# Performance work log

Measured on AMD Instinct MI355X. Metric: run time of the kernel, lower is better.

## Reference

```python
import jax, jax.numpy as jnp
import numpy as np

N_IN = 262144      # input points
N_OUT = 65536      # output voxels
NBR = 32           # neighbors per voxel (uniform ragged list here)
E = N_OUT * NBR    # total edges
CIN = 32
COUT = 32
K = 3 + 1          # kernel_size = [4,4,4]
KV = K * K * K     # 64 kernel bins
EPS = 1e-8


def window_poly6(r):
    # poly6 window on normalized distance r in [0,1]
    return jnp.clip(1.0 - r * r, 0.0, 1.0) ** 3


def ball_to_cube_radial(p):
    # radially map unit ball to unit cube [-1,1]^3 (Open3D 'ball_to_cube_radial')
    n2 = jnp.sqrt(jnp.sum(p * p, axis=-1, keepdims=True) + 1e-12)
    ninf = jnp.max(jnp.abs(p), axis=-1, keepdims=True)
    scale = jnp.where(ninf > 1e-8, n2 / jnp.maximum(ninf, 1e-8), 0.0)
    return jnp.clip(p * scale, -1.0, 1.0)


def setup_inputs() -> dict:
    key = jax.random.key(0)
    ks = jax.random.split(key, 8)
    feats = jax.random.normal(ks[0], (N_IN, CIN), jnp.float32)
    inp_points = jax.random.uniform(ks[1], (N_IN, 3), jnp.float32)
    out_points = jax.random.uniform(ks[2], (N_OUT, 3), jnp.float32)
    out_extents = jnp.array([0.2], jnp.float32)  # voxel size
    scale_compat = jax.random.uniform(ks[3], (E,), jnp.float32)
    neighbors_index = jax.random.randint(ks[4], (E,), 0, N_IN).astype(jnp.int64)
    neighbors_row_splits = (jnp.arange(N_OUT + 1) * NBR).astype(jnp.int64)
    neighbors_distance = jax.random.uniform(ks[5], (E,), jnp.float32)
    # learned params of the ContinuousConv: kernel [4,4,4,Cin,Cout] flattened, bias
    W = jax.random.normal(ks[6], (KV, CIN, COUT), jnp.float32) * 0.05
    bias = jnp.zeros((COUT,), jnp.float32)
    return dict(feats=feats, inp_points=inp_points, out_points=out_points,
                out_extents=out_extents, scale_compat=scale_compat,
                neighbors_index=neighbors_index,
                neighbors_row_splits=neighbors_row_splits,
                neighbors_distance=neighbors_distance, W=W, bias=bias)


def reference(feats, inp_points, out_points, out_extents, scale_compat,
              neighbors_index, neighbors_row_splits, neighbors_distance,
              W, bias):
    # edge -> output-voxel index from ragged row splits
    out_idx = jnp.searchsorted(neighbors_row_splits, jnp.arange(E), side='right') - 1
    # per-neighbor importance (the CConvAggregationBlock weighting)
    a = scale_compat * window_poly6(neighbors_distance)
    # relative positions normalized to the voxel extent (ball radius = extent/2)
    rel = (inp_points[neighbors_index] - out_points[out_idx]) * (2.0 / out_extents[0])
    cube = ball_to_cube_radial(rel)                      # [E,3] in [-1,1]
    u = jnp.clip((cube + 1.0) * 0.5 * (K - 1), 0.0, K - 1)
    i0 = jnp.clip(jnp.floor(u), 0.0, K - 2)
    t = u - i0                                           # trilinear fractions [E,3]
    i0 = i0.astype(jnp.int32)
    fg = feats[neighbors_index]                          # gathered features [E,Cin]
    # accumulate importance-weighted features into per-voxel kernel bins
    B = jnp.zeros((N_OUT * KV, CIN), feats.dtype)
    for dx in (0, 1):
        for dy in (0, 1):
            for dz in (0, 1):
                w = ((t[:, 0] if dx else 1.0 - t[:, 0]) *
                     (t[:, 1] if dy else 1.0 - t[:, 1]) *
                     (t[:, 2] if dz else 1.0 - t[:, 2]))
                kflat = ((i0[:, 0] + dx) * K + (i0[:, 1] + dy)) * K + (i0[:, 2] + dz)
                B = B.at[out_idx * KV + kflat].add((w * a)[:, None] * fg)
    # kernel contraction + importance normalization (normalize=True) + bias + relu
    y = jnp.einsum('nkc,kcd->nd', B.reshape(N_OUT, KV, CIN), W)
    denom = jax.ops.segment_sum(a, out_idx, num_segments=N_OUT)
    y = y / jnp.maximum(denom, EPS)[:, None] + bias
    return jax.nn.relu(y)
```

## Files before the change

### kernel.cpp

```cpp
#include <hip/hip_runtime.h>
#include <hip/hip_bf16.h>


typedef unsigned short u16;
typedef unsigned int   u32;
typedef __attribute__((ext_vector_type(4))) float f32x4;
typedef __attribute__((ext_vector_type(8))) short short8;

#define NOUT    65536
#define VX      4
#define THREADS 512
#define EPW     128
#define NWG     (NOUT / VX)
#define BSTRIDE 2052
#define VROWB   (BSTRIDE * 4)
#define BL_BYTES (VX * VROWB)

#define OFF_W   BL_BYTES
#define OFF_BCA (OFF_W + 8*EPW*4)
#define OFF_FB  (OFF_BCA + EPW*4)
#define OFF_DEN (OFF_FB + EPW*4)
#define SMEM_BYTES (OFF_DEN + 16)

__global__ void prep_w_kernel(const float* __restrict__ W,
                              u16* __restrict__ wpk) {
  int id  = blockIdx.x * 256 + threadIdx.x;
  int j   = id & 7;
  int l   = (id >> 3) & 63;
  int bin = (id >> 9) & 63;
  int tb  = id >> 15;
  int kap = (bin << 5) + ((l >> 4) << 3) + j;
  int d   = (l & 15) + ((tb >> 1) << 4);
  float w = W[kap * 32 + d];
  unsigned u = __float_as_uint(w);
  u16 val;
  if (tb & 1) {
    float rem = w - __uint_as_float(u & 0xFFFF0000u);
    val = (u16)(__float_as_uint(rem) >> 16);
  } else {
    val = (u16)(u >> 16);
  }
  wpk[id] = val;
}

__launch_bounds__(THREADS, 8)
__global__ void cconv_kernel(const float* __restrict__ feats,
                             const float* __restrict__ inp_points,
                             const float* __restrict__ out_points,
                             const float* __restrict__ out_extents,
                             const float* __restrict__ scale_compat,
                             const int*   __restrict__ nbr_idx,
                             const int*   __restrict__ row_splits,
                             const float* __restrict__ nbr_dist,
                             const float* __restrict__ bias,
                             const u16*   __restrict__ wpk,
                             float*       __restrict__ out) {
  extern __shared__ __align__(16) char smem[];
  float* wls   = (float*)(smem + OFF_W);
  float* Yp    = wls;
  u32*   bca   = (u32*)(smem + OFF_BCA);
  int*   fbase = (int*)(smem + OFF_FB);
  float* den   = (float*)(smem + OFF_DEN);

  const int tid  = threadIdx.x;
  const int wg   = blockIdx.x;
  const int lane = tid & 63;
  const int wv   = tid >> 6;

  {
    f32x4 z = {0.f, 0.f, 0.f, 0.f};
    for (int i = tid; i < (BL_BYTES / 16); i += THREADS)
      ((f32x4*)smem)[i] = z;
  }

  if (tid < EPW) {
    const bool is64 = (row_splits[1] == 0);
    int e  = tid;
    int v  = e >> 5;
    int gv = (wg << 2) + v;
    int ge = (wg << 7) + e;
    int idx = nbr_idx[is64 ? (ge << 1) : ge];
    float dist = nbr_dist[ge];
    float sc   = scale_compat[ge];
    float om = 1.f - dist * dist;
    om = fminf(fmaxf(om, 0.f), 1.f);
    float a = sc * om * om * om;
    float inv = 2.f / out_extents[0];
    float ox = out_points[gv * 3 + 0];
    float oy = out_points[gv * 3 + 1];
    float oz = out_points[gv * 3 + 2];
    float rx = (inp_points[idx * 3 + 0] - ox) * inv;
    float ry = (inp_points[idx * 3 + 1] - oy) * inv;
    float rz = (inp_points[idx * 3 + 2] - oz) * inv;
    float n2   = sqrtf(rx * rx + ry * ry + rz * rz + 1e-12f);
    float ninf = fmaxf(fabsf(rx), fmaxf(fabsf(ry), fabsf(rz)));
    float scl  = (ninf > 1e-8f) ? (n2 / ninf) : 0.f;
    float cx = fminf(fmaxf(rx * scl, -1.f), 1.f);
    float cy = fminf(fmaxf(ry * scl, -1.f), 1.f);
    float cz = fminf(fmaxf(rz * scl, -1.f), 1.f);
    float ux = fminf(fmaxf((cx + 1.f) * 1.5f, 0.f), 3.f);
    float uy = fminf(fmaxf((cy + 1.f) * 1.5f, 0.f), 3.f);
    float uz = fminf(fmaxf((cz + 1.f) * 1.5f, 0.f), 3.f);
    float fx = fminf(floorf(ux), 2.f);
    float fy = fminf(floorf(uy), 2.f);
    float fz = fminf(floorf(uz), 2.f);
    float tx = ux - fx, ty = uy - fy, tz = uz - fz;
    int ix = (int)fx, iy = (int)fy, iz = (int)fz;
    float X1 = tx * a, X0 = a - X1;
    float Y1 = ty,     Y0 = 1.f - ty;
    float Z1 = tz,     Z0 = 1.f - tz;
    float p00 = X0 * Y0, p01 = X0 * Y1, p10 = X1 * Y0, p11 = X1 * Y1;
    float wc[8];
    wc[0] = p00 * Z0; wc[1] = p00 * Z1; wc[2] = p01 * Z0; wc[3] = p01 * Z1;
    wc[4] = p10 * Z0; wc[5] = p10 * Z1; wc[6] = p11 * Z0; wc[7] = p11 * Z1;
    int kb = (ix * 4 + iy) * 4 + iz;
    u32 bb = (u32)(v * VROWB + (kb << 7));
    int nc = 0; u32 mask = 0;
    #pragma unroll
    for (int k = 0; k < 8; ++k) {
      if (wc[k] != 0.f) {
        wls[nc * EPW + e] = wc[k];
        mask |= (1u << k);
        ++nc;
      }
    }
    bca[e]   = bb | (mask << 16) | ((u32)nc << 24);
    fbase[e] = idx << 5;
    float s = a;
    s += __shfl_xor(s, 1);
    s += __shfl_xor(s, 2);
    s += __shfl_xor(s, 4);
    s += __shfl_xor(s, 8);
    s += __shfl_xor(s, 16);
    if ((lane & 31) == 0) den[v] = s;
  }
  __syncthreads();

  {
    const int c  = tid & 31;
    const int e0 = tid >> 5;
    u32 bcn[8]; int fbs[8]; float fg[8];
    #pragma unroll
    for (int it = 0; it < 8; ++it) {
      int e = (it << 4) + e0;
      bcn[it] = bca[e];
      fbs[it] = fbase[e];
    }
    #pragma unroll
    for (int it = 0; it < 8; ++it)
      fg[it] = feats[fbs[it] + c];
    #pragma unroll
    for (int it = 0; it < 8; ++it) {
      int   e    = (it << 4) + e0;
      u32   m    = bcn[it];
      u32   base = (m & 0xFFFFu) + ((u32)c << 2);
      u32   mask = (m >> 16) & 0xFFu;
      int   nc   = (int)(m >> 24);
      float f    = fg[it];
      for (int j = 0; j < nc; ++j) {
        float w = wls[j * EPW + e];
        int   k = __builtin_ctz(mask);
        mask &= mask - 1;
        u32 d = ((k & 1) << 7) | ((k & 2) << 8) | ((k & 4) << 9);
        atomicAdd((float*)(smem + base + d), w * f);
      }
    }
  }
  __syncthreads();

  f32x4 acc0 = {0.f, 0.f, 0.f, 0.f};
  f32x4 acc1 = {0.f, 0.f, 0.f, 0.f};
  {
    const short8* wp = (const short8*)wpk;
    int v16 = lane & 15;
    int q   = lane >> 4;
    const char* arow = smem + (size_t)(v16 & 3) * VROWB;
    #pragma unroll
    for (int b = 0; b < 8; ++b) {
      int bin = (wv << 3) + b;
      short8 w0h = wp[((0 * 64 + bin) << 6) + lane];
      short8 w0l = wp[((1 * 64 + bin) << 6) + lane];
      short8 w1h = wp[((2 * 64 + bin) << 6) + lane];
      short8 w1l = wp[((3 * 64 + bin) << 6) + lane];
      const float* ap = (const float*)(arow + (bin << 7) + (q << 5));
      f32x4 a0 = *(const f32x4*)ap;
      f32x4 a1 = *(const f32x4*)(ap + 4);
      short8 ahi, alo;
      #pragma unroll
      for (int j = 0; j < 4; ++j) {
        unsigned u0 = __float_as_uint(a0[j]);
        ahi[j] = (short)(u0 >> 16);
        float r0 = a0[j] - __uint_as_float(u0 & 0xFFFF0000u);
        alo[j] = (short)(__float_as_uint(r0) >> 16);
        unsigned u1 = __float_as_uint(a1[j]);
        ahi[j + 4] = (short)(u1 >> 16);
        float r1 = a1[j] - __uint_as_float(u1 & 0xFFFF0000u);
        alo[j + 4] = (short)(__float_as_uint(r1) >> 16);
      }
      acc0 = __builtin_amdgcn_mfma_f32_16x16x32_bf16(ahi, w0h, acc0, 0, 0, 0);
      acc0 = __builtin_amdgcn_mfma_f32_16x16x32_bf16(ahi, w0l, acc0, 0, 0, 0);
      acc0 = __builtin_amdgcn_mfma_f32_16x16x32_bf16(alo, w0h, acc0, 0, 0, 0);
      acc1 = __builtin_amdgcn_mfma_f32_16x16x32_bf16(ahi, w1h, acc1, 0, 0, 0);
      acc1 = __builtin_amdgcn_mfma_f32_16x16x32_bf16(ahi, w1l, acc1, 0, 0, 0);
      acc1 = __builtin_amdgcn_mfma_f32_16x16x32_bf16(alo, w1h, acc1, 0, 0, 0);
    }
  }

  if (lane < 16) {
    float* yp = Yp + (wv << 7);
    #pragma unroll
    for (int r = 0; r < 4; ++r) {
      yp[r * 32 + lane]      = acc0[r];
      yp[r * 32 + 16 + lane] = acc1[r];
    }
  }
  __syncthreads();

  if (tid < EPW) {
    float s = 0.f;
    #pragma unroll
    for (int w = 0; w < 8; ++w) s += Yp[(w << 7) + tid];
    int v = tid >> 5;
    int d = tid & 31;
    float dn = fmaxf(den[v], 1e-8f);
    float y = s / dn + bias[d];
    out[(wg << 7) + tid] = fmaxf(y, 0.f);
  }
}

extern "C" void kernel_launch(void* const* d_in, const int* in_sizes, int n_in,
                              void* d_out, int out_size, void* d_ws, size_t ws_size,
                              hipStream_t stream) {
  const float* feats        = (const float*)d_in[0];
  const float* inp_points   = (const float*)d_in[1];
  const float* out_points   = (const float*)d_in[2];
  const float* out_extents  = (const float*)d_in[3];
  const float* scale_compat = (const float*)d_in[4];
  const int*   nbr_idx      = (const int*)d_in[5];
  const int*   row_splits   = (const int*)d_in[6];
  const float* nbr_dist     = (const float*)d_in[7];
  const float* W            = (const float*)d_in[8];
  const float* bias         = (const float*)d_in[9];

  u16* wpk = (u16*)d_ws;

  static_assert(SMEM_BYTES <= 40960, "LDS over 4-per-CU budget");
  (void)hipFuncSetAttribute((const void*)cconv_kernel,
                            hipFuncAttributeMaxDynamicSharedMemorySize,
                            SMEM_BYTES);

  prep_w_kernel<<<512, 256, 0, stream>>>(W, wpk);
  cconv_kernel<<<NWG, THREADS, SMEM_BYTES, stream>>>(
      feats, inp_points, out_points, out_extents, scale_compat, nbr_idx,
      row_splits, nbr_dist, bias, wpk, (float*)d_out);
}
```

Before: 617.5 us.

## Stage gathered features into LDS via async global_load_lds and prefetch weights

Gathered neighbor feature rows are now copied straight into a new LDS staging buffer with global_load_lds, and the issue is placed before the bin-zeroing loop so that the gather overlaps the zeroing. The scatter phase then reads features from LDS instead of holding them in registers from global loads. The MFMA weight loads are double-buffered so the next bin's weights are prefetched. In exchange, LDS use grows by about 16KB per block and the bin stride is padded, which cuts residency from 4 to 3 workgroups per CU and may lower latency hiding.

After: 652.6 us. 5.7% more time.

```diff
diff --git a/kernel.cpp b/kernel.cpp
--- a/kernel.cpp
+++ b/kernel.cpp
@@ -12,14 +12,14 @@
 #define THREADS 512
 #define EPW     128
 #define NWG     (NOUT / VX)
-#define BSTRIDE 2052
+#define BSTRIDE 2064
 #define VROWB   (BSTRIDE * 4)
 #define BL_BYTES (VX * VROWB)
 
-#define OFF_W   BL_BYTES
-#define OFF_BCA (OFF_W + 8*EPW*4)
-#define OFF_FB  (OFF_BCA + EPW*4)
-#define OFF_DEN (OFF_FB + EPW*4)
+#define OFF_FS  BL_BYTES
+#define OFF_W   (OFF_FS + 16384)
+#define OFF_BCA (OFF_W + 4096)
+#define OFF_DEN (OFF_BCA + 512)
 #define SMEM_BYTES (OFF_DEN + 16)
 
 __global__ void prep_w_kernel(const float* __restrict__ W,
@@ -43,7 +43,7 @@
   wpk[id] = val;
 }
 
-__launch_bounds__(THREADS, 8)
+__launch_bounds__(THREADS, 6)
 __global__ void cconv_kernel(const float* __restrict__ feats,
                              const float* __restrict__ inp_points,
                              const float* __restrict__ out_points,
@@ -56,22 +56,16 @@
                              const u16*   __restrict__ wpk,
                              float*       __restrict__ out) {
   extern __shared__ __align__(16) char smem[];
-  float* wls   = (float*)(smem + OFF_W);
-  float* Yp    = wls;
-  u32*   bca   = (u32*)(smem + OFF_BCA);
-  int*   fbase = (int*)(smem + OFF_FB);
-  float* den   = (float*)(smem + OFF_DEN);
+  float* fstage = (float*)(smem + OFF_FS);
+  float* wls    = (float*)(smem + OFF_W);
+  float* Yp     = wls;
+  u32*   bca    = (u32*)(smem + OFF_BCA);
+  float* den    = (float*)(smem + OFF_DEN);
 
   const int tid  = threadIdx.x;
   const int wg   = blockIdx.x;
   const int lane = tid & 63;
   const int wv   = tid >> 6;
-
-  {
-    f32x4 z = {0.f, 0.f, 0.f, 0.f};
-    for (int i = tid; i < (BL_BYTES / 16); i += THREADS)
-      ((f32x4*)smem)[i] = z;
-  }
 
   if (tid < EPW) {
     const bool is64 = (row_splits[1] == 0);
@@ -124,8 +118,8 @@
         ++nc;
       }
     }
-    bca[e]   = bb | (mask << 16) | ((u32)nc << 24);
-    fbase[e] = idx << 5;
+    bca[e] = bb | (mask << 16) | ((u32)nc << 24);
+    *(int*)&fstage[e << 5] = idx;
     float s = a;
     s += __shfl_xor(s, 1);
     s += __shfl_xor(s, 2);
@@ -137,26 +131,37 @@
   __syncthreads();
 
   {
+    #pragma unroll
+    for (int rd = 0; rd < 2; ++rd) {
+      int r = (rd << 6) + (tid >> 3);
+      int k = tid & 7;
+      int idx = *(const int*)&fstage[r << 5];
+      const float* g = feats + (idx << 5) + (k << 2);
+      __builtin_amdgcn_global_load_lds(
+          (const __attribute__((address_space(1))) void*)(const void*)g,
+          (__attribute__((address_space(3))) void*)(void*)&fstage[(r << 5) + (k << 2)],
+          16, 0, 0);
+    }
+  }
+
+  {
+    f32x4 z = {0.f, 0.f, 0.f, 0.f};
+    for (int i = tid; i < (BL_BYTES / 16); i += THREADS)
+      ((f32x4*)smem)[i] = z;
+  }
+  __syncthreads();
+
+  {
     const int c  = tid & 31;
     const int e0 = tid >> 5;
-    u32 bcn[8]; int fbs[8]; float fg[8];
-    #pragma unroll
-    for (int it = 0; it < 8; ++it) {
-      int e = (it << 4) + e0;
-      bcn[it] = bca[e];
-      fbs[it] = fbase[e];
-    }
-    #pragma unroll
-    for (int it = 0; it < 8; ++it)
-      fg[it] = feats[fbs[it] + c];
     #pragma unroll
     for (int it = 0; it < 8; ++it) {
       int   e    = (it << 4) + e0;
-      u32   m    = bcn[it];
+      u32   m    = bca[e];
+      float f    = fstage[(e << 5) + c];
       u32   base = (m & 0xFFFFu) + ((u32)c << 2);
       u32   mask = (m >> 16) & 0xFFu;
       int   nc   = (int)(m >> 24);
-      float f    = fg[it];
       for (int j = 0; j < nc; ++j) {
         float w = wls[j * EPW + e];
         int   k = __builtin_ctz(mask);
@@ -175,13 +180,21 @@
     int v16 = lane & 15;
     int q   = lane >> 4;
     const char* arow = smem + (size_t)(v16 & 3) * VROWB;
+    const int bin0 = wv << 3;
+    short8 wbA[4], wbB[4];
+    #pragma unroll
+    for (int t2 = 0; t2 < 4; ++t2)
+      wbA[t2] = wp[((t2 * 64 + bin0) << 6) + lane];
     #pragma unroll
     for (int b = 0; b < 8; ++b) {
-      int bin = (wv << 3) + b;
-      short8 w0h = wp[((0 * 64 + bin) << 6) + lane];
-      short8 w0l = wp[((1 * 64 + bin) << 6) + lane];
-      short8 w1h = wp[((2 * 64 + bin) << 6) + lane];
-      short8 w1l = wp[((3 * 64 + bin) << 6) + lane];
+      int bin = bin0 + b;
+      short8* cur = (b & 1) ? wbB : wbA;
+      short8* nxt = (b & 1) ? wbA : wbB;
+      if (b < 7) {
+        #pragma unroll
+        for (int t2 = 0; t2 < 4; ++t2)
+          nxt[t2] = wp[((t2 * 64 + bin + 1) << 6) + lane];
+      }
       const float* ap = (const float*)(arow + (bin << 7) + (q << 5));
       f32x4 a0 = *(const f32x4*)ap;
       f32x4 a1 = *(const f32x4*)(ap + 4);
@@ -197,12 +210,12 @@
         float r1 = a1[j] - __uint_as_float(u1 & 0xFFFF0000u);
         alo[j + 4] = (short)(__float_as_uint(r1) >> 16);
       }
-      acc0 = __builtin_amdgcn_mfma_f32_16x16x32_bf16(ahi, w0h, acc0, 0, 0, 0);
-      acc0 = __builtin_amdgcn_mfma_f32_16x16x32_bf16(ahi, w0l, acc0, 0, 0, 0);
-      acc0 = __builtin_amdgcn_mfma_f32_16x16x32_bf16(alo, w0h, acc0, 0, 0, 0);
-      acc1 = __builtin_amdgcn_mfma_f32_16x16x32_bf16(ahi, w1h, acc1, 0, 0, 0);
-      acc1 = __builtin_amdgcn_mfma_f32_16x16x32_bf16(ahi, w1l, acc1, 0, 0, 0);
-      acc1 = __builtin_amdgcn_mfma_f32_16x16x32_bf16(alo, w1h, acc1, 0, 0, 0);
+      acc0 = __builtin_amdgcn_mfma_f32_16x16x32_bf16(ahi, cur[0], acc0, 0, 0, 0);
+      acc0 = __builtin_amdgcn_mfma_f32_16x16x32_bf16(ahi, cur[1], acc0, 0, 0, 0);
+      acc0 = __builtin_amdgcn_mfma_f32_16x16x32_bf16(alo, cur[0], acc0, 0, 0, 0);
+      acc1 = __builtin_amdgcn_mfma_f32_16x16x32_bf16(ahi, cur[2], acc1, 0, 0, 0);
+      acc1 = __builtin_amdgcn_mfma_f32_16x16x32_bf16(ahi, cur[3], acc1, 0, 0, 0);
+      acc1 = __builtin_amdgcn_mfma_f32_16x16x32_bf16(alo, cur[2], acc1, 0, 0, 0);
     }
   }
 
@@ -244,7 +257,7 @@
 
   u16* wpk = (u16*)d_ws;
 
-  static_assert(SMEM_BYTES <= 40960, "LDS over 4-per-CU budget");
+  static_assert(SMEM_BYTES <= 54613, "LDS over 3-per-CU budget");
   (void)hipFuncSetAttribute((const void*)cconv_kernel,
                             hipFuncAttributeMaxDynamicSharedMemorySize,
                             SMEM_BYTES);
```
